# Kernel tuning notes

Measured on AMD Instinct MI355X. Metric: run time of the kernel, lower is better.

Reference implementation:

```python
import jax, jax.numpy as jnp
import numpy as np


def setup_inputs() -> dict:
    key = jax.random.key(0)
    k1, k2 = jax.random.split(key)
    B, D, H, W = 16, 64, 64, 64
    K = 1024  # codebook_size
    x = jax.random.normal(k1, (B, D, H, W), dtype=jnp.float32)
    codebook = jax.random.normal(k2, (K, D), dtype=jnp.float32)
    return {"x": x, "codebook": codebook}


def reference(x, codebook):
    """VQ quantization: nearest-codebook lookup.

    x: (B, D, H, W) latent features; codebook: (K, D).
    Returns (quantized (B, D, H, W), indices (B, H, W)).
    """
    B, D, H, W = x.shape
    # (B, D, H, W) -> (B*H*W, D)
    flat = jnp.transpose(x, (0, 2, 3, 1)).reshape(-1, D)
    d2 = (
        jnp.sum(flat * flat, axis=-1, keepdims=True)
        - 2.0 * (flat @ codebook.T)
        + jnp.sum(codebook * codebook, axis=-1)
    )
    idx = jnp.argmin(d2, axis=-1)  # (N,)
    quantized = codebook[idx]  # (N, D) gather
    quantized = quantized.reshape(B, H, W, D).transpose(0, 3, 1, 2)
    return quantized, idx.reshape(B, H, W)
```

## Files before the change

### kernel.cpp

```cpp
#include <hip/hip_runtime.h>
#include <hip/hip_bf16.h>

#define D_ 64
#define HW_ 4096
#define K_ 1024
#define NPTS_ 65536
#define QOUT_ 4194304
#define DELTA 0.006f
#define INF_ 3.4e38f
#define NCH 32

typedef short bf16x8 __attribute__((ext_vector_type(8)));
typedef float f32x4 __attribute__((ext_vector_type(4)));

__device__ __forceinline__ void gload_lds16(const float* g, float* l) {
    __builtin_amdgcn_global_load_lds((const __attribute__((address_space(1))) void*)g,
                                     (__attribute__((address_space(3))) void*)l, 16, 0, 0);
}

__global__ __launch_bounds__(256) void vq_pack(const float* __restrict__ cb,
                                               float* __restrict__ cnorm,
                                               short* __restrict__ P) {
    const int t = blockIdx.x * 256 + threadIdx.x;
    const int gch = t >> 6, l = t & 63;
    const int j  = gch * 16 + (l & 15);
    const int dg = l >> 4;
#pragma unroll
    for (int s = 0; s < 2; ++s) {
        const float* src = cb + j * D_ + s * 32 + dg * 8;
        short hb[8], lb[8];
#pragma unroll
        for (int i = 0; i < 8; ++i) {
            const float v = -2.f * src[i];
            __hip_bfloat16 h = __float2bfloat16(v);
            hb[i] = *(const short*)&h;
            const float r = v - __bfloat162float(h);
            __hip_bfloat16 lo = __float2bfloat16(r);
            lb[i] = *(const short*)&lo;
        }
        short* dh = P + ((size_t)(gch * 4 + s * 2 + 0) * 64 + l) * 8;
        short* dl = P + ((size_t)(gch * 4 + s * 2 + 1) * 64 + l) * 8;
#pragma unroll
        for (int i = 0; i < 8; ++i) { dh[i] = hb[i]; dl[i] = lb[i]; }
    }
    if (t < K_) {
        const float4* r = (const float4*)(cb + (size_t)t * D_);
        float s0 = 0.f, s1 = 0.f, s2 = 0.f, s3 = 0.f;
#pragma unroll
        for (int i = 0; i < 16; ++i) {
            float4 v = r[i];
            s0 = fmaf(v.x, v.x, s0); s1 = fmaf(v.y, v.y, s1);
            s2 = fmaf(v.z, v.z, s2); s3 = fmaf(v.w, v.w, s3);
        }
        cnorm[t] = (s0 + s1) + (s2 + s3);
    }
}

__device__ __forceinline__ void stage_chunk(const float* src, float* dst,
                                            int wid, int lane) {
#pragma unroll
    for (int r = 0; r < 2; ++r)
        gload_lds16(src + (wid * 2 + r) * 256 + lane * 4,
                    dst + (wid * 2 + r) * 256);
}

__global__ __launch_bounds__(256, 4) void vq_main(const float* __restrict__ x,
                                                  const float* __restrict__ cb,
                                                  const float* __restrict__ cnorm_g,
                                                  const short* __restrict__ P,
                                                  float* __restrict__ out) {
    __shared__ short cbuf[3][4096];
    __shared__ float cnt[K_];
    __shared__ int res_idx[64];
    __shared__ int flist[64];
    __shared__ int fcnt;

    const int tid  = threadIdx.x;
    const int lane = tid & 63;
    const int wid  = tid >> 6;
    const int pg   = blockIdx.x;
    const int bb   = pg >> 6;
    const int hw0  = (pg & 63) << 6;

    if (tid == 0) fcnt = 0;

    const float* Pf = (const float*)P;
    float* buf0 = (float*)cbuf[0];
    float* buf1 = (float*)cbuf[1];
    float* buf2 = (float*)cbuf[2];

    gload_lds16(cnorm_g + wid * 256 + lane * 4, cnt + wid * 256);
    stage_chunk(Pf, buf0, wid, lane);
    stage_chunk(Pf + 2048, buf1, wid, lane);

    bf16x8 ah[2], al[2];
    {
        const float* xb = x + (size_t)bb * (D_ * HW_) + hw0;
        const int p_l = wid * 16 + (lane & 15);
#pragma unroll
        for (int s = 0; s < 2; ++s) {
            const int d0 = s * 32 + (lane >> 4) * 8;
#pragma unroll
            for (int i = 0; i < 8; ++i) {
                const float v = xb[(size_t)(d0 + i) * HW_ + p_l];
                __hip_bfloat16 h = __float2bfloat16(v);
                ah[s][i] = *(const short*)&h;
                const float r = v - __bfloat162float(h);
                __hip_bfloat16 lo = __float2bfloat16(r);
                al[s][i] = *(const short*)&lo;
            }
        }
    }
    asm volatile("s_waitcnt vmcnt(2)" ::: "memory");
    __builtin_amdgcn_s_barrier();
    asm volatile("" ::: "memory");

    float m1[4], m2[4];
    int   i1[4];
#pragma unroll
    for (int q = 0; q < 4; ++q) { m1[q] = INF_; m2[q] = INF_; i1[q] = 0; }

    float* bcur = buf0;
    float* bnxt = buf1;
    float* bstg = buf2;
#pragma unroll 1
    for (int c = 0; c < NCH; ++c) {
        if (c + 2 < NCH) stage_chunk(Pf + (size_t)(c + 2) * 2048, bstg, wid, lane);

        const bf16x8* fr = (const bf16x8*)bcur;
#pragma unroll
        for (int gl = 0; gl < 2; ++gl) {
            const int kc = c * 32 + gl * 16 + (lane & 15);
            const float cn = cnt[kc];
            bf16x8 bh0 = fr[(gl * 4 + 0) * 64 + lane];
            bf16x8 bl0 = fr[(gl * 4 + 1) * 64 + lane];
            bf16x8 bh1 = fr[(gl * 4 + 2) * 64 + lane];
            bf16x8 bl1 = fr[(gl * 4 + 3) * 64 + lane];
            f32x4 aa = {0.f, 0.f, 0.f, 0.f};
            f32x4 ab = {0.f, 0.f, 0.f, 0.f};
            aa = __builtin_amdgcn_mfma_f32_16x16x32_bf16(ah[0], bh0, aa, 0, 0, 0);
            ab = __builtin_amdgcn_mfma_f32_16x16x32_bf16(ah[1], bh1, ab, 0, 0, 0);
            aa = __builtin_amdgcn_mfma_f32_16x16x32_bf16(al[0], bh0, aa, 0, 0, 0);
            ab = __builtin_amdgcn_mfma_f32_16x16x32_bf16(al[1], bh1, ab, 0, 0, 0);
            aa = __builtin_amdgcn_mfma_f32_16x16x32_bf16(ah[0], bl0, aa, 0, 0, 0);
            ab = __builtin_amdgcn_mfma_f32_16x16x32_bf16(ah[1], bl1, ab, 0, 0, 0);
#pragma unroll
            for (int r = 0; r < 4; ++r) {
                const float d2 = cn + (aa[r] + ab[r]);
                const bool lt = d2 < m1[r];
                m2[r] = fminf(m2[r], fmaxf(m1[r], d2));
                m1[r] = fminf(m1[r], d2);
                i1[r] = lt ? kc : i1[r];
            }
        }

        if (c + 2 < NCH) asm volatile("s_waitcnt vmcnt(2)" ::: "memory");
        else             asm volatile("s_waitcnt vmcnt(0)" ::: "memory");
        __builtin_amdgcn_s_barrier();
        asm volatile("" ::: "memory");

        float* t0 = bcur; bcur = bnxt; bnxt = bstg; bstg = t0;
    }

#pragma unroll
    for (int q = 0; q < 4; ++q) {
        float a1 = m1[q], a2 = m2[q];
        int   ai = i1[q];
#pragma unroll
        for (int m = 1; m < 16; m <<= 1) {
            const float o1 = __shfl_xor(a1, m);
            const int   oi = __shfl_xor(ai, m);
            const float o2 = __shfl_xor(a2, m);
            const float nm2 = fminf(fminf(a2, o2), fmaxf(a1, o1));
            if (o1 < a1 || (o1 == a1 && oi < ai)) { a1 = o1; ai = oi; }
            a2 = nm2;
        }
        if ((lane & 15) == 0) {
            const int pt = wid * 16 + 4 * (lane >> 4) + q;
            res_idx[pt] = ai;
            if (a2 - a1 <= DELTA) { const int p = atomicAdd(&fcnt, 1); flist[p] = pt; }
        }
    }
    __syncthreads();

    const int nf = fcnt;
    for (int i = wid; i < nf; i += 4) {
        const int pt = flist[i];
        const float* xr = x + (size_t)bb * (D_ * HW_) + hw0 + pt;
        float xv[D_];
#pragma unroll
        for (int d = 0; d < D_; ++d) xv[d] = xr[(size_t)d * HW_];
        float b1 = INF_; int bi = 0;
        for (int cc = 0; cc < 16; ++cc) {
            const int row = lane * 16 + cc;
            const float4* cr = (const float4*)(cb + (size_t)row * D_);
            float a0 = 0.f, a1 = 0.f, a2 = 0.f, a3 = 0.f;
#pragma unroll
            for (int g = 0; g < 16; ++g) {
                const float4 cf = cr[g];
                a0 = fmaf(xv[4 * g + 0], cf.x, a0);
                a1 = fmaf(xv[4 * g + 1], cf.y, a1);
                a2 = fmaf(xv[4 * g + 2], cf.z, a2);
                a3 = fmaf(xv[4 * g + 3], cf.w, a3);
            }
            const float dot = (a0 + a1) + (a2 + a3);
            const float d2 = fmaf(-2.f, dot, cnt[row]);
            if (d2 < b1) { b1 = d2; bi = row; }
        }
#pragma unroll
        for (int m = 1; m < 64; m <<= 1) {
            const float o1 = __shfl_xor(b1, m);
            const int   oi = __shfl_xor(bi, m);
            if (o1 < b1 || (o1 == b1 && oi < bi)) { b1 = o1; bi = oi; }
        }
        if (lane == 0) res_idx[pt] = bi;
    }
    __syncthreads();

    if (tid < 64) out[(size_t)QOUT_ + (pg << 6) + tid] = (float)res_idx[tid];

    float* tile = (float*)cbuf;
#pragma unroll
    for (int pass = 0; pass < 4; ++pass) {
        const int pl = pass * 16 + (tid >> 4);
        const int dq = tid & 15;
        const float4 v = *(const float4*)(cb + (size_t)res_idx[pl] * D_ + dq * 4);
        tile[pl * 65 + dq * 4 + 0] = v.x;
        tile[pl * 65 + dq * 4 + 1] = v.y;
        tile[pl * 65 + dq * 4 + 2] = v.z;
        tile[pl * 65 + dq * 4 + 3] = v.w;
    }
    __syncthreads();
    float* ob = out + (size_t)bb * (D_ * HW_) + hw0;
#pragma unroll
    for (int it = 0; it < 4; ++it) {
        const int e = it * 256 + tid;
        const int d = e >> 4;
        const int g = e & 15;
        float4 q;
        q.x = tile[(g * 4 + 0) * 65 + d];
        q.y = tile[(g * 4 + 1) * 65 + d];
        q.z = tile[(g * 4 + 2) * 65 + d];
        q.w = tile[(g * 4 + 3) * 65 + d];
        *(float4*)(ob + (size_t)d * HW_ + g * 4) = q;
    }
}

extern "C" void kernel_launch(void* const* d_in, const int* in_sizes, int n_in,
                              void* d_out, int out_size, void* d_ws, size_t ws_size,
                              hipStream_t stream) {
    const float* x  = (const float*)d_in[0];
    const float* cb = (const float*)d_in[1];
    float* out   = (float*)d_out;
    float* cnorm = (float*)d_ws;
    short* P     = (short*)((char*)d_ws + 4096);

    vq_pack<<<16, 256, 0, stream>>>(cb, cnorm, P);
    vq_main<<<NPTS_ / 64, 256, 0, stream>>>(x, cb, cnorm, P, out);
}
```

Before: 69.68 us.

## Split gather into separate kernel and use double-buffered LDS staging

Moves the quantized-output gather and transpose out of the main kernel into a separate vq_write kernel. That kernel reads the indices back from the output buffer and gathers codebook entries per element. The main kernel drops from a triple-buffered LDS pipeline with fine-grained vmcnt waits to a double-buffered one with full __syncthreads, which cuts LDS use. The pack kernel now runs with 64-thread blocks. The costs are an extra launch, a round trip of the indices through global memory, and less latency hiding in the codebook streaming loop.

```diff
diff --git a/kernel.cpp b/kernel.cpp
--- a/kernel.cpp
+++ b/kernel.cpp
@@ -18,10 +18,10 @@
                                      (__attribute__((address_space(3))) void*)l, 16, 0, 0);
 }
 
-__global__ __launch_bounds__(256) void vq_pack(const float* __restrict__ cb,
-                                               float* __restrict__ cnorm,
-                                               short* __restrict__ P) {
-    const int t = blockIdx.x * 256 + threadIdx.x;
+__global__ __launch_bounds__(64) void vq_pack(const float* __restrict__ cb,
+                                              float* __restrict__ cnorm,
+                                              short* __restrict__ P) {
+    const int t = blockIdx.x * 64 + threadIdx.x;
     const int gch = t >> 6, l = t & 63;
     const int j  = gch * 16 + (l & 15);
     const int dg = l >> 4;
@@ -56,20 +56,12 @@
     }
 }
 
-__device__ __forceinline__ void stage_chunk(const float* src, float* dst,
-                                            int wid, int lane) {
-#pragma unroll
-    for (int r = 0; r < 2; ++r)
-        gload_lds16(src + (wid * 2 + r) * 256 + lane * 4,
-                    dst + (wid * 2 + r) * 256);
-}
-
 __global__ __launch_bounds__(256, 4) void vq_main(const float* __restrict__ x,
                                                   const float* __restrict__ cb,
                                                   const float* __restrict__ cnorm_g,
                                                   const short* __restrict__ P,
                                                   float* __restrict__ out) {
-    __shared__ short cbuf[3][4096];
+    __shared__ short cbuf[2][4096];
     __shared__ float cnt[K_];
     __shared__ int res_idx[64];
     __shared__ int flist[64];
@@ -85,13 +77,12 @@
     if (tid == 0) fcnt = 0;
 
     const float* Pf = (const float*)P;
-    float* buf0 = (float*)cbuf[0];
-    float* buf1 = (float*)cbuf[1];
-    float* buf2 = (float*)cbuf[2];
 
     gload_lds16(cnorm_g + wid * 256 + lane * 4, cnt + wid * 256);
-    stage_chunk(Pf, buf0, wid, lane);
-    stage_chunk(Pf + 2048, buf1, wid, lane);
+#pragma unroll
+    for (int r = 0; r < 2; ++r)
+        gload_lds16(Pf + (wid * 2 + r) * 256 + lane * 4,
+                    (float*)cbuf[0] + (wid * 2 + r) * 256);
 
     bf16x8 ah[2], al[2];
     {
@@ -111,31 +102,34 @@
             }
         }
     }
-    asm volatile("s_waitcnt vmcnt(2)" ::: "memory");
-    __builtin_amdgcn_s_barrier();
-    asm volatile("" ::: "memory");
+    asm volatile("s_waitcnt vmcnt(0)" ::: "memory");
+    __syncthreads();
 
     float m1[4], m2[4];
     int   i1[4];
 #pragma unroll
     for (int q = 0; q < 4; ++q) { m1[q] = INF_; m2[q] = INF_; i1[q] = 0; }
 
-    float* bcur = buf0;
-    float* bnxt = buf1;
-    float* bstg = buf2;
+    int cur = 0;
 #pragma unroll 1
     for (int c = 0; c < NCH; ++c) {
-        if (c + 2 < NCH) stage_chunk(Pf + (size_t)(c + 2) * 2048, bstg, wid, lane);
-
-        const bf16x8* fr = (const bf16x8*)bcur;
-#pragma unroll
-        for (int gl = 0; gl < 2; ++gl) {
-            const int kc = c * 32 + gl * 16 + (lane & 15);
+        if (c + 1 < NCH) {
+            const float* src = Pf + (size_t)(c + 1) * 2048;
+            float* dst = (float*)cbuf[cur ^ 1];
+#pragma unroll
+            for (int r = 0; r < 2; ++r)
+                gload_lds16(src + (wid * 2 + r) * 256 + lane * 4,
+                            dst + (wid * 2 + r) * 256);
+        }
+        const bf16x8* fr = (const bf16x8*)cbuf[cur];
+#pragma unroll
+        for (int u = 0; u < 2; ++u) {
+            const int kc = c * 32 + u * 16 + (lane & 15);
             const float cn = cnt[kc];
-            bf16x8 bh0 = fr[(gl * 4 + 0) * 64 + lane];
-            bf16x8 bl0 = fr[(gl * 4 + 1) * 64 + lane];
-            bf16x8 bh1 = fr[(gl * 4 + 2) * 64 + lane];
-            bf16x8 bl1 = fr[(gl * 4 + 3) * 64 + lane];
+            bf16x8 bh0 = fr[(u * 4 + 0) * 64 + lane];
+            bf16x8 bl0 = fr[(u * 4 + 1) * 64 + lane];
+            bf16x8 bh1 = fr[(u * 4 + 2) * 64 + lane];
+            bf16x8 bl1 = fr[(u * 4 + 3) * 64 + lane];
             f32x4 aa = {0.f, 0.f, 0.f, 0.f};
             f32x4 ab = {0.f, 0.f, 0.f, 0.f};
             aa = __builtin_amdgcn_mfma_f32_16x16x32_bf16(ah[0], bh0, aa, 0, 0, 0);
@@ -153,13 +147,8 @@
                 i1[r] = lt ? kc : i1[r];
             }
         }
-
-        if (c + 2 < NCH) asm volatile("s_waitcnt vmcnt(2)" ::: "memory");
-        else             asm volatile("s_waitcnt vmcnt(0)" ::: "memory");
-        __builtin_amdgcn_s_barrier();
-        asm volatile("" ::: "memory");
-
-        float* t0 = bcur; bcur = bnxt; bnxt = bstg; bstg = t0;
+        __syncthreads();
+        cur ^= 1;
     }
 
 #pragma unroll
@@ -218,32 +207,22 @@
     __syncthreads();
 
     if (tid < 64) out[(size_t)QOUT_ + (pg << 6) + tid] = (float)res_idx[tid];
-
-    float* tile = (float*)cbuf;
-#pragma unroll
-    for (int pass = 0; pass < 4; ++pass) {
-        const int pl = pass * 16 + (tid >> 4);
-        const int dq = tid & 15;
-        const float4 v = *(const float4*)(cb + (size_t)res_idx[pl] * D_ + dq * 4);
-        tile[pl * 65 + dq * 4 + 0] = v.x;
-        tile[pl * 65 + dq * 4 + 1] = v.y;
-        tile[pl * 65 + dq * 4 + 2] = v.z;
-        tile[pl * 65 + dq * 4 + 3] = v.w;
-    }
-    __syncthreads();
-    float* ob = out + (size_t)bb * (D_ * HW_) + hw0;
-#pragma unroll
-    for (int it = 0; it < 4; ++it) {
-        const int e = it * 256 + tid;
-        const int d = e >> 4;
-        const int g = e & 15;
-        float4 q;
-        q.x = tile[(g * 4 + 0) * 65 + d];
-        q.y = tile[(g * 4 + 1) * 65 + d];
-        q.z = tile[(g * 4 + 2) * 65 + d];
-        q.w = tile[(g * 4 + 3) * 65 + d];
-        *(float4*)(ob + (size_t)d * HW_ + g * 4) = q;
-    }
+}
+
+__global__ __launch_bounds__(256) void vq_write(const float* __restrict__ cb,
+                                                float* __restrict__ out) {
+    const int e = blockIdx.x * 256 + threadIdx.x;
+    const int b = e >> 16;
+    const int r = e & 65535;
+    const int d = r >> 10;
+    const int g = r & 1023;
+    const float4 fi = *(const float4*)(out + (size_t)QOUT_ + b * HW_ + g * 4);
+    float4 q;
+    q.x = cb[(size_t)((int)fi.x) * D_ + d];
+    q.y = cb[(size_t)((int)fi.y) * D_ + d];
+    q.z = cb[(size_t)((int)fi.z) * D_ + d];
+    q.w = cb[(size_t)((int)fi.w) * D_ + d];
+    *(float4*)(out + ((size_t)b * D_ + d) * HW_ + g * 4) = q;
 }
 
 extern "C" void kernel_launch(void* const* d_in, const int* in_sizes, int n_in,
@@ -255,6 +234,7 @@
     float* cnorm = (float*)d_ws;
     short* P     = (short*)((char*)d_ws + 4096);
 
-    vq_pack<<<16, 256, 0, stream>>>(cb, cnorm, P);
+    vq_pack<<<64, 64, 0, stream>>>(cb, cnorm, P);
     vq_main<<<NPTS_ / 64, 256, 0, stream>>>(x, cb, cnorm, P, out);
-}
+    vq_write<<<(NPTS_ * D_ / 4) / 256, 256, 0, stream>>>(cb, out);
+}
```

New measurement: 79.93 us. 1.15x slower.
